# Kernel optimization log

Hardware: AMD Instinct MI355X
Metric: run time of the kernel (lower is better)

The kernel has to match this reference:

```python
import jax, jax.numpy as jnp
import numpy as np

B, N, D, H = 8, 1024, 512, 512  # batch, nodes/graph, input dim, hidden/output dim
NEG_SLOPE = 0.2


def _gatv2_layer(x, src, dst, Wl, bl, Wr, br, a, bias, nseg):
    """PyG GATv2Conv (heads=1, add_self_loops=False, eval mode -> no dropout).
    message j->i: alpha_ij = softmax_i( a . leaky_relu(xl[j] + xr[i]) ); out[i] = sum_j alpha_ij * xl[j] + bias
    """
    xl = x @ Wl + bl              # [nseg, H] source transform
    xr = x @ Wr + br              # [nseg, H] target transform
    e = jax.nn.leaky_relu(xl[src] + xr[dst], NEG_SLOPE) @ a  # [E] raw scores
    m = jax.lax.stop_gradient(jax.ops.segment_max(e, dst, num_segments=nseg))
    ex = jnp.exp(e - m[dst])
    s = jax.ops.segment_sum(ex, dst, num_segments=nseg)
    alpha = ex / s[dst]                                       # segment softmax over incoming edges
    out = jax.ops.segment_sum(alpha[:, None] * xl[src], dst, num_segments=nseg)
    return out + bias


def setup_inputs() -> dict:
    key = jax.random.key(0)
    rng = np.random.RandomState(0)
    # random per-graph adjacency, avg degree ~16; block-diagonal edge extraction
    adj_np = (rng.rand(B, N, N) < (16.0 / N))
    srcs, dsts = [], []
    for b in range(B):  # matches torch.nonzero(big_adj).t(): row=src, col=dst
        r, c = np.nonzero(adj_np[b])
        srcs.append(r + b * N)
        dsts.append(c + b * N)
    edge_index = jnp.asarray(np.stack([np.concatenate(srcs), np.concatenate(dsts)]).astype(np.int32))

    ks = jax.random.split(key, 32)
    def lin(k, fi, fo):
        return (jax.random.normal(k, (fi, fo), jnp.float32) / np.sqrt(fi)).astype(jnp.float32)
    inp = {
        "batch_graph": jax.random.normal(ks[0], (B, N, D), jnp.float32),
        "adj": jnp.asarray(adj_np.astype(np.float32)),
        "edge_index": edge_index,
    }
    dims = [(D, H), (H, H), (H, H)]
    for i, (fi, fo) in enumerate(dims, start=1):
        k = jax.random.split(ks[i], 6)
        inp[f"Wl{i}"] = lin(k[0], fi, fo)
        inp[f"bl{i}"] = jnp.zeros((fo,), jnp.float32)
        inp[f"Wr{i}"] = lin(k[1], fi, fo)
        inp[f"br{i}"] = jnp.zeros((fo,), jnp.float32)
        inp[f"a{i}"] = (jax.random.normal(k[2], (fo,), jnp.float32) / np.sqrt(fo)).astype(jnp.float32)
        inp[f"bias{i}"] = jnp.zeros((fo,), jnp.float32)
    return inp


def reference(batch_graph, adj, edge_index,
              Wl1, bl1, Wr1, br1, a1, bias1,
              Wl2, bl2, Wr2, br2, a2, bias2,
              Wl3, bl3, Wr3, br3, a3, bias3):
    b, n, d = batch_graph.shape
    nseg = b * n
    x = batch_graph.reshape(nseg, d)
    src, dst = edge_index[0], edge_index[1]
    x = _gatv2_layer(x, src, dst, Wl1, bl1, Wr1, br1, a1, bias1, nseg)  # graph_norm = Identity
    x = _gatv2_layer(x, src, dst, Wl2, bl2, Wr2, br2, a2, bias2, nseg)
    x = _gatv2_layer(x, src, dst, Wl3, bl3, Wr3, br3, a3, bias3, nseg)
    return x.reshape(b, n, -1)
```

## Files before the change

### kernel.cpp

```cpp
#include <hip/hip_runtime.h>
#include <math.h>

#define MTOT 8192
#define HD   512

typedef __attribute__((ext_vector_type(8))) short bf16x8;
typedef __attribute__((ext_vector_type(4))) float floatx4;

__device__ inline unsigned short f2bf(float f) {
    unsigned int u = __float_as_uint(f);
    unsigned int r = (u + 0x7FFFu + ((u >> 16) & 1u)) >> 16;
    return (unsigned short)r;
}
__device__ inline float bf2f(unsigned short h) {
    return __uint_as_float(((unsigned int)h) << 16);
}

__device__ inline float wave_sum64(float v) {
    int t;
    t = __builtin_amdgcn_update_dpp(0, __float_as_int(v), 0x121, 0xF, 0xF, true); v += __int_as_float(t);
    t = __builtin_amdgcn_update_dpp(0, __float_as_int(v), 0x122, 0xF, 0xF, true); v += __int_as_float(t);
    t = __builtin_amdgcn_update_dpp(0, __float_as_int(v), 0x124, 0xF, 0xF, true); v += __int_as_float(t);
    t = __builtin_amdgcn_update_dpp(0, __float_as_int(v), 0x128, 0xF, 0xF, true); v += __int_as_float(t);
    v += __shfl_xor(v, 16, 64);
    v += __shfl_xor(v, 32, 64);
    return v;
}


__global__ void count_deg(const int* __restrict__ dst, int* __restrict__ deg, int E) {
    int i = blockIdx.x * 256 + threadIdx.x;
    if (i < E) atomicAdd(&deg[dst[i]], 1);
}

__global__ __launch_bounds__(1024) void scan_offsets(const int* __restrict__ deg,
                                                     int* __restrict__ offs,
                                                     int* __restrict__ cursor) {
    __shared__ int part[1024];
    int tid = threadIdx.x;
    int base = tid * 8;
    int v[8]; int s = 0;
    #pragma unroll
    for (int i = 0; i < 8; ++i) { v[i] = deg[base + i]; s += v[i]; }
    part[tid] = s;
    __syncthreads();
    for (int off = 1; off < 1024; off <<= 1) {
        int t = (tid >= off) ? part[tid - off] : 0;
        __syncthreads();
        part[tid] += t;
        __syncthreads();
    }
    int run = (tid == 0) ? 0 : part[tid - 1];
    #pragma unroll
    for (int i = 0; i < 8; ++i) {
        offs[base + i] = run;
        cursor[base + i] = run;
        run += v[i];
    }
    if (tid == 1023) offs[MTOT] = run;
}

__global__ void scatter_edges(const int* __restrict__ src, const int* __restrict__ dst,
                              int* __restrict__ cursor, int* __restrict__ csr_src, int E) {
    int i = blockIdx.x * 256 + threadIdx.x;
    if (i < E) {
        int p = atomicAdd(&cursor[dst[i]], 1);
        csr_src[p] = src[i];
    }
}


__global__ __launch_bounds__(256) void prep_convert(
    const float* __restrict__ W0, const float* __restrict__ W1,
    const float* __restrict__ W2, const float* __restrict__ W3,
    const float* __restrict__ W4, const float* __restrict__ W5,
    unsigned short* __restrict__ wtbase,
    const float* __restrict__ X,
    unsigned short* __restrict__ Ahi, unsigned short* __restrict__ Alo,
    int* __restrict__ deg)
{
    int z = blockIdx.z;
    if (z == 7) {
        if (blockIdx.x == 0 && blockIdx.y == 0)
            for (int i = threadIdx.x; i < MTOT; i += 256) deg[i] = 0;
        return;
    }
    if (z == 6) {
        int bid = blockIdx.x * 16 + blockIdx.y;
        int t0 = bid * 256 + threadIdx.x;
        #pragma unroll
        for (int it = 0; it < 16; ++it) {
            int i = (t0 + it * 65536) * 4;
            float4 vv = *(const float4*)(X + i);
            ushort4 h, l;
            h.x = f2bf(vv.x); l.x = f2bf(vv.x - bf2f(h.x));
            h.y = f2bf(vv.y); l.y = f2bf(vv.y - bf2f(h.y));
            h.z = f2bf(vv.z); l.z = f2bf(vv.z - bf2f(h.z));
            h.w = f2bf(vv.w); l.w = f2bf(vv.w - bf2f(h.w));
            *(ushort4*)(Ahi + i) = h;
            *(ushort4*)(Alo + i) = l;
        }
        return;
    }
    const float* W = (z == 0) ? W0 : (z == 1) ? W1 : (z == 2) ? W2
                   : (z == 3) ? W3 : (z == 4) ? W4 : W5;
    int L = z >> 1, lr = z & 1;
    const size_t SZ = (size_t)HD * HD;
    unsigned short* Whi = wtbase + (L * 4 + lr * 2) * SZ;
    unsigned short* Wlo = Whi + SZ;

    __shared__ float t[32][33];
    int bx = blockIdx.x * 32;
    int by = blockIdx.y * 32;
    int tx = threadIdx.x & 31, ty = threadIdx.x >> 5;
    for (int i = ty; i < 32; i += 8)
        t[i][tx] = W[(size_t)(by + i) * HD + bx + tx];
    __syncthreads();
    for (int i = ty; i < 32; i += 8) {
        float vv = t[tx][i];
        unsigned short h = f2bf(vv);
        unsigned short l = f2bf(vv - bf2f(h));
        Whi[(size_t)(bx + i) * HD + by + tx] = h;
        Wlo[(size_t)(bx + i) * HD + by + tx] = l;
    }
}


__global__ __launch_bounds__(256) void gemm_mfma_dual(
    const unsigned short* __restrict__ Ahi, const unsigned short* __restrict__ Alo,
    const unsigned short* __restrict__ Bhi_l, const unsigned short* __restrict__ Blo_l,
    const unsigned short* __restrict__ Bhi_r, const unsigned short* __restrict__ Blo_r,
    const float* __restrict__ bias_l, const float* __restrict__ bias_r,
    float* __restrict__ Cl, float* __restrict__ Cr)
{
    int bid = blockIdx.x;
    int virt = (bid & 7) * 64 + (bid >> 3);
    int g  = virt >> 3;
    int q  = virt & 7;
    int bz = q >> 2;
    int bm = g * 128, bn = (q & 3) * 128;

    const unsigned short* Bhi = bz ? Bhi_r : Bhi_l;
    const unsigned short* Blo = bz ? Blo_r : Blo_l;
    const float* bias         = bz ? bias_r : bias_l;
    float* C                  = bz ? Cr : Cl;

    __shared__ __align__(16) unsigned short lds[2][4 * 128 * 32];

    int tid = threadIdx.x;
    int wave = tid >> 6, lane = tid & 63;

    const unsigned short* gsrc[4] = {Ahi, Alo, Bhi, Blo};
    int rowbase[4] = {bm, bm, bn, bn};

    const unsigned short* gbase =
        gsrc[wave] + (size_t)(rowbase[wave] + (lane >> 2)) * 512 + (lane & 3) * 8;

    floatx4 acc[4][4] = {};

    int wm = wave & 1, wn = wave >> 1;
    int lr = lane & 15, lq = lane >> 4;

    #pragma unroll
    for (int rg = 0; rg < 8; ++rg) {
        __builtin_amdgcn_global_load_lds(
            (const __attribute__((address_space(1))) unsigned int*)(gbase + (size_t)rg * 16 * 512),
            (__attribute__((address_space(3))) unsigned int*)(&lds[0][wave * 4096 + rg * 512]),
            16, 0, 0);
    }
    __syncthreads();

    for (int it = 0; it < 16; ++it) {
        int cur = it & 1;
        if (it < 15) {
            const unsigned short* g2 = gbase + (it + 1) * 32;
            #pragma unroll
            for (int rg = 0; rg < 8; ++rg) {
                __builtin_amdgcn_global_load_lds(
                    (const __attribute__((address_space(1))) unsigned int*)(g2 + (size_t)rg * 16 * 512),
                    (__attribute__((address_space(3))) unsigned int*)(&lds[cur ^ 1][wave * 4096 + rg * 512]),
                    16, 0, 0);
            }
        }

        bf16x8 ah[4], al[4], bh[4], bl_[4];
        #pragma unroll
        for (int i = 0; i < 4; ++i) {
            int mrow = wm * 64 + i * 16 + lr;
            ah[i]  = *(const bf16x8*)&lds[cur][0 * 4096 + mrow * 32 + lq * 8];
            al[i]  = *(const bf16x8*)&lds[cur][1 * 4096 + mrow * 32 + lq * 8];
            int nrow = wn * 64 + i * 16 + lr;
            bh[i]  = *(const bf16x8*)&lds[cur][2 * 4096 + nrow * 32 + lq * 8];
            bl_[i] = *(const bf16x8*)&lds[cur][3 * 4096 + nrow * 32 + lq * 8];
        }
        #pragma unroll
        for (int i = 0; i < 4; ++i)
            #pragma unroll
            for (int j = 0; j < 4; ++j) {
                acc[i][j] = __builtin_amdgcn_mfma_f32_16x16x32_bf16(ah[i], bh[j],  acc[i][j], 0, 0, 0);
                acc[i][j] = __builtin_amdgcn_mfma_f32_16x16x32_bf16(ah[i], bl_[j], acc[i][j], 0, 0, 0);
                acc[i][j] = __builtin_amdgcn_mfma_f32_16x16x32_bf16(al[i], bh[j],  acc[i][j], 0, 0, 0);
            }

        __syncthreads();
    }

    #pragma unroll
    for (int j = 0; j < 4; ++j) {
        int n = bn + wn * 64 + j * 16 + lr;
        float bv = bias[n];
        #pragma unroll
        for (int i = 0; i < 4; ++i) {
            int mbase = bm + wm * 64 + i * 16 + lq * 4;
            #pragma unroll
            for (int r = 0; r < 4; ++r)
                C[(size_t)(mbase + r) * 512 + n] = acc[i][j][r] + bv;
        }
    }
}


#define DOT8(Xa, Xb, d0, d1)                                              \
    {                                                                     \
        float t_;                                                         \
        t_ = Xa.x + r0.x; d0 = fmaf(av0.x, t_, d0); d1 = fmaf(av0.x, fabsf(t_), d1); \
        t_ = Xa.y + r0.y; d0 = fmaf(av0.y, t_, d0); d1 = fmaf(av0.y, fabsf(t_), d1); \
        t_ = Xa.z + r0.z; d0 = fmaf(av0.z, t_, d0); d1 = fmaf(av0.z, fabsf(t_), d1); \
        t_ = Xa.w + r0.w; d0 = fmaf(av0.w, t_, d0); d1 = fmaf(av0.w, fabsf(t_), d1); \
        t_ = Xb.x + r1.x; d0 = fmaf(av1.x, t_, d0); d1 = fmaf(av1.x, fabsf(t_), d1); \
        t_ = Xb.y + r1.y; d0 = fmaf(av1.y, t_, d0); d1 = fmaf(av1.y, fabsf(t_), d1); \
        t_ = Xb.z + r1.z; d0 = fmaf(av1.z, t_, d0); d1 = fmaf(av1.z, fabsf(t_), d1); \
        t_ = Xb.w + r1.w; d0 = fmaf(av1.w, t_, d0); d1 = fmaf(av1.w, fabsf(t_), d1); \
    }

#define PROCESS4(Xa, Xb, q)                                               \
    {                                                                     \
        float pe[4];                                                      \
        _Pragma("unroll")                                                 \
        for (int k2 = 0; k2 < 4; ++k2) {                                  \
            float d0 = 0.f, d1 = 0.f;                                     \
            DOT8(Xa[k2], Xb[k2], d0, d1);                                 \
            pe[k2] = fmaf(0.6f, d0, 0.4f * d1);                           \
        }                                                                 \
        _Pragma("unroll")                                                 \
        for (int k2 = 0; k2 < 4; ++k2) pe[k2] = wave_sum64(pe[k2]);       \
        float e0 = pe[0];                                                 \
        float e1 = ((q) + 1 < ne) ? pe[1] : -3.0e38f;                     \
        float e2 = ((q) + 2 < ne) ? pe[2] : -3.0e38f;                     \
        float e3 = ((q) + 3 < ne) ? pe[3] : -3.0e38f;                     \
        float bm4 = fmaxf(fmaxf(e0, e1), fmaxf(e2, e3));                  \
        if (bm4 > m) {                                                    \
            float sc = __expf(m - bm4);                                   \
            s *= sc;                                                      \
            acc0.x *= sc; acc0.y *= sc; acc0.z *= sc; acc0.w *= sc;       \
            acc1.x *= sc; acc1.y *= sc; acc1.z *= sc; acc1.w *= sc;       \
            m = bm4;                                                      \
        }                                                                 \
        float w0 = __expf(e0 - m), w1 = __expf(e1 - m);                   \
        float w2 = __expf(e2 - m), w3 = __expf(e3 - m);                   \
        s += (w0 + w1) + (w2 + w3);                                       \
        acc0.x = fmaf(w0, Xa[0].x, fmaf(w1, Xa[1].x, fmaf(w2, Xa[2].x, fmaf(w3, Xa[3].x, acc0.x)))); \
        acc0.y = fmaf(w0, Xa[0].y, fmaf(w1, Xa[1].y, fmaf(w2, Xa[2].y, fmaf(w3, Xa[3].y, acc0.y)))); \
        acc0.z = fmaf(w0, Xa[0].z, fmaf(w1, Xa[1].z, fmaf(w2, Xa[2].z, fmaf(w3, Xa[3].z, acc0.z)))); \
        acc0.w = fmaf(w0, Xa[0].w, fmaf(w1, Xa[1].w, fmaf(w2, Xa[2].w, fmaf(w3, Xa[3].w, acc0.w)))); \
        acc1.x = fmaf(w0, Xb[0].x, fmaf(w1, Xb[1].x, fmaf(w2, Xb[2].x, fmaf(w3, Xb[3].x, acc1.x)))); \
        acc1.y = fmaf(w0, Xb[0].y, fmaf(w1, Xb[1].y, fmaf(w2, Xb[2].y, fmaf(w3, Xb[3].y, acc1.y)))); \
        acc1.z = fmaf(w0, Xb[0].z, fmaf(w1, Xb[1].z, fmaf(w2, Xb[2].z, fmaf(w3, Xb[3].z, acc1.z)))); \
        acc1.w = fmaf(w0, Xb[0].w, fmaf(w1, Xb[1].w, fmaf(w2, Xb[2].w, fmaf(w3, Xb[3].w, acc1.w)))); \
    }

__global__ __launch_bounds__(256, 4) void gat_online(
    const float* __restrict__ xl, const float* __restrict__ xr,
    const float* __restrict__ avec, const float* __restrict__ bias,
    const int* __restrict__ offs, const int* __restrict__ csr_src,
    float* __restrict__ out, unsigned short* __restrict__ Ohi,
    unsigned short* __restrict__ Olo, int write_fp32)
{
    int gid = blockIdx.x;
    int wv = threadIdx.x >> 6, lane = threadIdx.x & 63;
    int node = ((gid & 7) << 10) + ((gid >> 3) << 2) + wv;

    int nb = offs[node], ne = offs[node + 1];

    int jA[4], jB[4];
    int j0 = (nb < ne) ? csr_src[nb] : 0;
    jA[0] = j0;
    #pragma unroll
    for (int k = 1; k < 4; ++k) jA[k] = (nb + k < ne) ? csr_src[nb + k] : j0;
    #pragma unroll
    for (int k = 0; k < 4; ++k) jB[k] = (nb + 4 + k < ne) ? csr_src[nb + 4 + k] : j0;

    size_t loff = (size_t)lane * 8;
    size_t rowoff = (size_t)node * HD + loff;
    float4 r0 = *(const float4*)(xr + rowoff);
    float4 r1 = *(const float4*)(xr + rowoff + 4);
    float4 av0 = *(const float4*)(avec + loff);
    float4 av1 = *(const float4*)(avec + loff + 4);

    float m = -3.0e38f, s = 0.f;
    float4 acc0 = {0.f, 0.f, 0.f, 0.f}, acc1 = {0.f, 0.f, 0.f, 0.f};

    float4 Aa[4], Ab[4], Ba[4], Bb[4];
    #pragma unroll
    for (int k = 0; k < 4; ++k) {
        const float* xp = xl + (size_t)jA[k] * HD + loff;
        Aa[k] = *(const float4*)xp;
        Ab[k] = *(const float4*)(xp + 4);
    }

    int p = nb;
    if (p < ne) {
        for (;;) {
            #pragma unroll
            for (int k = 0; k < 4; ++k) {
                const float* xp = xl + (size_t)jB[k] * HD + loff;
                Ba[k] = *(const float4*)xp;
                Bb[k] = *(const float4*)(xp + 4);
            }
            {
                int p2 = p + 8;
                #pragma unroll
                for (int k = 0; k < 4; ++k)
                    jA[k] = (p2 + k < ne) ? csr_src[p2 + k] : j0;
            }
            PROCESS4(Aa, Ab, p);
            p += 4;
            if (p >= ne) break;

            #pragma unroll
            for (int k = 0; k < 4; ++k) {
                const float* xp = xl + (size_t)jA[k] * HD + loff;
                Aa[k] = *(const float4*)xp;
                Ab[k] = *(const float4*)(xp + 4);
            }
            {
                int p2 = p + 8;
                #pragma unroll
                for (int k = 0; k < 4; ++k)
                    jB[k] = (p2 + k < ne) ? csr_src[p2 + k] : j0;
            }
            PROCESS4(Ba, Bb, p);
            p += 4;
            if (p >= ne) break;
        }
    }

    float inv = (s > 0.f) ? 1.f / s : 0.f;
    float4 b0 = *(const float4*)(bias + loff);
    float4 b1 = *(const float4*)(bias + loff + 4);
    float4 o0, o1;
    o0.x = fmaf(acc0.x, inv, b0.x); o0.y = fmaf(acc0.y, inv, b0.y);
    o0.z = fmaf(acc0.z, inv, b0.z); o0.w = fmaf(acc0.w, inv, b0.w);
    o1.x = fmaf(acc1.x, inv, b1.x); o1.y = fmaf(acc1.y, inv, b1.y);
    o1.z = fmaf(acc1.z, inv, b1.z); o1.w = fmaf(acc1.w, inv, b1.w);

    if (write_fp32) {
        *(float4*)(out + rowoff) = o0;
        *(float4*)(out + rowoff + 4) = o1;
    } else {
        ushort4 h, lo;
        h.x = f2bf(o0.x); lo.x = f2bf(o0.x - bf2f(h.x));
        h.y = f2bf(o0.y); lo.y = f2bf(o0.y - bf2f(h.y));
        h.z = f2bf(o0.z); lo.z = f2bf(o0.z - bf2f(h.z));
        h.w = f2bf(o0.w); lo.w = f2bf(o0.w - bf2f(h.w));
        *(ushort4*)(Ohi + rowoff) = h;
        *(ushort4*)(Olo + rowoff) = lo;
        h.x = f2bf(o1.x); lo.x = f2bf(o1.x - bf2f(h.x));
        h.y = f2bf(o1.y); lo.y = f2bf(o1.y - bf2f(h.y));
        h.z = f2bf(o1.z); lo.z = f2bf(o1.z - bf2f(h.z));
        h.w = f2bf(o1.w); lo.w = f2bf(o1.w - bf2f(h.w));
        *(ushort4*)(Ohi + rowoff + 4) = h;
        *(ushort4*)(Olo + rowoff + 4) = lo;
    }
}


extern "C" void kernel_launch(void* const* d_in, const int* in_sizes, int n_in,
                              void* d_out, int out_size, void* d_ws, size_t ws_size,
                              hipStream_t stream) {
    const float* x0 = (const float*)d_in[0];
    const int* eidx = (const int*)d_in[2];
    int E = in_sizes[2] / 2;
    const int* esrc = eidx;
    const int* edst = eidx + E;

    const float* Wl[3] = {(const float*)d_in[3],  (const float*)d_in[9],  (const float*)d_in[15]};
    const float* bl[3] = {(const float*)d_in[4],  (const float*)d_in[10], (const float*)d_in[16]};
    const float* Wr[3] = {(const float*)d_in[5],  (const float*)d_in[11], (const float*)d_in[17]};
    const float* br[3] = {(const float*)d_in[6],  (const float*)d_in[12], (const float*)d_in[18]};
    const float* av[3] = {(const float*)d_in[7],  (const float*)d_in[13], (const float*)d_in[19]};
    const float* bs[3] = {(const float*)d_in[8],  (const float*)d_in[14], (const float*)d_in[20]};

    char* w = (char*)d_ws;
    unsigned short* Ahi = (unsigned short*)w; w += (size_t)MTOT * HD * 2;
    unsigned short* Alo = (unsigned short*)w; w += (size_t)MTOT * HD * 2;
    unsigned short* wtbase = (unsigned short*)w; w += 12 * (size_t)HD * HD * 2;
    float* xl = (float*)w; w += (size_t)MTOT * HD * 4;
    float* xr = (float*)w; w += (size_t)MTOT * HD * 4;
    int* deg    = (int*)w;
    int* offs   = deg + MTOT;
    int* cursor = offs + MTOT + 8;
    int* csr    = cursor + MTOT;
    const size_t SZ = (size_t)HD * HD;

    prep_convert<<<dim3(16, 16, 8), 256, 0, stream>>>(
        Wl[0], Wr[0], Wl[1], Wr[1], Wl[2], Wr[2], wtbase, x0, Ahi, Alo, deg);
    count_deg<<<(E + 255) / 256, 256, 0, stream>>>(edst, deg, E);
    scan_offsets<<<1, 1024, 0, stream>>>(deg, offs, cursor);
    scatter_edges<<<(E + 255) / 256, 256, 0, stream>>>(esrc, edst, cursor, csr, E);

    for (int L = 0; L < 3; ++L) {
        gemm_mfma_dual<<<512, 256, 0, stream>>>(Ahi, Alo,
            wtbase + (L * 4 + 0) * SZ, wtbase + (L * 4 + 1) * SZ,
            wtbase + (L * 4 + 2) * SZ, wtbase + (L * 4 + 3) * SZ,
            bl[L], br[L], xl, xr);
        int last = (L == 2);
        gat_online<<<MTOT / 4, 256, 0, stream>>>(xl, xr, av[L], bs[L], offs, csr,
                                                 last ? (float*)d_out : nullptr,
                                                 last ? nullptr : Ahi,
                                                 last ? nullptr : Alo,
                                                 last);
    }
}
```

Measured before the change: 305.7 us.

## Process two destination nodes per wave in GAT aggregation, interleaving their edge streams

The online-softmax aggregation kernel now assigns two destination nodes to each wave instead of one, alternating 4-edge chunks between the two nodes so that one node's gathers can overlap the other's compute. The grid is halved and the launch-bounds occupancy hint drops from 4 to 3 to allow for the extra registers. Each node's prefetch is now single-buffered rather than double-buffered, and the added register pressure lowers occupancy, which may cancel the gain from the added instruction-level parallelism.

```diff
diff --git a/kernel.cpp b/kernel.cpp
--- a/kernel.cpp
+++ b/kernel.cpp
@@ -220,56 +220,84 @@
 }
 
 
-#define DOT8(Xa, Xb, d0, d1)                                              \
+#define DOT8P(Xa, Xb, Ra, Rb, d0, d1)                                     \
     {                                                                     \
         float t_;                                                         \
-        t_ = Xa.x + r0.x; d0 = fmaf(av0.x, t_, d0); d1 = fmaf(av0.x, fabsf(t_), d1); \
-        t_ = Xa.y + r0.y; d0 = fmaf(av0.y, t_, d0); d1 = fmaf(av0.y, fabsf(t_), d1); \
-        t_ = Xa.z + r0.z; d0 = fmaf(av0.z, t_, d0); d1 = fmaf(av0.z, fabsf(t_), d1); \
-        t_ = Xa.w + r0.w; d0 = fmaf(av0.w, t_, d0); d1 = fmaf(av0.w, fabsf(t_), d1); \
-        t_ = Xb.x + r1.x; d0 = fmaf(av1.x, t_, d0); d1 = fmaf(av1.x, fabsf(t_), d1); \
-        t_ = Xb.y + r1.y; d0 = fmaf(av1.y, t_, d0); d1 = fmaf(av1.y, fabsf(t_), d1); \
-        t_ = Xb.z + r1.z; d0 = fmaf(av1.z, t_, d0); d1 = fmaf(av1.z, fabsf(t_), d1); \
-        t_ = Xb.w + r1.w; d0 = fmaf(av1.w, t_, d0); d1 = fmaf(av1.w, fabsf(t_), d1); \
-    }
-
-#define PROCESS4(Xa, Xb, q)                                               \
+        t_ = Xa.x + Ra.x; d0 = fmaf(av0.x, t_, d0); d1 = fmaf(av0.x, fabsf(t_), d1); \
+        t_ = Xa.y + Ra.y; d0 = fmaf(av0.y, t_, d0); d1 = fmaf(av0.y, fabsf(t_), d1); \
+        t_ = Xa.z + Ra.z; d0 = fmaf(av0.z, t_, d0); d1 = fmaf(av0.z, fabsf(t_), d1); \
+        t_ = Xa.w + Ra.w; d0 = fmaf(av0.w, t_, d0); d1 = fmaf(av0.w, fabsf(t_), d1); \
+        t_ = Xb.x + Rb.x; d0 = fmaf(av1.x, t_, d0); d1 = fmaf(av1.x, fabsf(t_), d1); \
+        t_ = Xb.y + Rb.y; d0 = fmaf(av1.y, t_, d0); d1 = fmaf(av1.y, fabsf(t_), d1); \
+        t_ = Xb.z + Rb.z; d0 = fmaf(av1.z, t_, d0); d1 = fmaf(av1.z, fabsf(t_), d1); \
+        t_ = Xb.w + Rb.w; d0 = fmaf(av1.w, t_, d0); d1 = fmaf(av1.w, fabsf(t_), d1); \
+    }
+
+#define PROC4(Xa, Xb, q, NE, M, S, A0, A1, Ra, Rb)                        \
     {                                                                     \
         float pe[4];                                                      \
         _Pragma("unroll")                                                 \
         for (int k2 = 0; k2 < 4; ++k2) {                                  \
             float d0 = 0.f, d1 = 0.f;                                     \
-            DOT8(Xa[k2], Xb[k2], d0, d1);                                 \
+            DOT8P(Xa[k2], Xb[k2], Ra, Rb, d0, d1);                        \
             pe[k2] = fmaf(0.6f, d0, 0.4f * d1);                           \
         }                                                                 \
         _Pragma("unroll")                                                 \
         for (int k2 = 0; k2 < 4; ++k2) pe[k2] = wave_sum64(pe[k2]);       \
         float e0 = pe[0];                                                 \
-        float e1 = ((q) + 1 < ne) ? pe[1] : -3.0e38f;                     \
-        float e2 = ((q) + 2 < ne) ? pe[2] : -3.0e38f;                     \
-        float e3 = ((q) + 3 < ne) ? pe[3] : -3.0e38f;                     \
+        float e1 = ((q) + 1 < (NE)) ? pe[1] : -3.0e38f;                   \
+        float e2 = ((q) + 2 < (NE)) ? pe[2] : -3.0e38f;                   \
+        float e3 = ((q) + 3 < (NE)) ? pe[3] : -3.0e38f;                   \
         float bm4 = fmaxf(fmaxf(e0, e1), fmaxf(e2, e3));                  \
-        if (bm4 > m) {                                                    \
-            float sc = __expf(m - bm4);                                   \
-            s *= sc;                                                      \
-            acc0.x *= sc; acc0.y *= sc; acc0.z *= sc; acc0.w *= sc;       \
-            acc1.x *= sc; acc1.y *= sc; acc1.z *= sc; acc1.w *= sc;       \
-            m = bm4;                                                      \
+        if (bm4 > (M)) {                                                  \
+            float sc = __expf((M) - bm4);                                 \
+            (S) *= sc;                                                    \
+            A0.x *= sc; A0.y *= sc; A0.z *= sc; A0.w *= sc;               \
+            A1.x *= sc; A1.y *= sc; A1.z *= sc; A1.w *= sc;               \
+            (M) = bm4;                                                    \
         }                                                                 \
-        float w0 = __expf(e0 - m), w1 = __expf(e1 - m);                   \
-        float w2 = __expf(e2 - m), w3 = __expf(e3 - m);                   \
-        s += (w0 + w1) + (w2 + w3);                                       \
-        acc0.x = fmaf(w0, Xa[0].x, fmaf(w1, Xa[1].x, fmaf(w2, Xa[2].x, fmaf(w3, Xa[3].x, acc0.x)))); \
-        acc0.y = fmaf(w0, Xa[0].y, fmaf(w1, Xa[1].y, fmaf(w2, Xa[2].y, fmaf(w3, Xa[3].y, acc0.y)))); \
-        acc0.z = fmaf(w0, Xa[0].z, fmaf(w1, Xa[1].z, fmaf(w2, Xa[2].z, fmaf(w3, Xa[3].z, acc0.z)))); \
-        acc0.w = fmaf(w0, Xa[0].w, fmaf(w1, Xa[1].w, fmaf(w2, Xa[2].w, fmaf(w3, Xa[3].w, acc0.w)))); \
-        acc1.x = fmaf(w0, Xb[0].x, fmaf(w1, Xb[1].x, fmaf(w2, Xb[2].x, fmaf(w3, Xb[3].x, acc1.x)))); \
-        acc1.y = fmaf(w0, Xb[0].y, fmaf(w1, Xb[1].y, fmaf(w2, Xb[2].y, fmaf(w3, Xb[3].y, acc1.y)))); \
-        acc1.z = fmaf(w0, Xb[0].z, fmaf(w1, Xb[1].z, fmaf(w2, Xb[2].z, fmaf(w3, Xb[3].z, acc1.z)))); \
-        acc1.w = fmaf(w0, Xb[0].w, fmaf(w1, Xb[1].w, fmaf(w2, Xb[2].w, fmaf(w3, Xb[3].w, acc1.w)))); \
-    }
-
-__global__ __launch_bounds__(256, 4) void gat_online(
+        float w0 = __expf(e0 - (M)), w1 = __expf(e1 - (M));               \
+        float w2 = __expf(e2 - (M)), w3 = __expf(e3 - (M));               \
+        (S) += (w0 + w1) + (w2 + w3);                                     \
+        A0.x = fmaf(w0, Xa[0].x, fmaf(w1, Xa[1].x, fmaf(w2, Xa[2].x, fmaf(w3, Xa[3].x, A0.x)))); \
+        A0.y = fmaf(w0, Xa[0].y, fmaf(w1, Xa[1].y, fmaf(w2, Xa[2].y, fmaf(w3, Xa[3].y, A0.y)))); \
+        A0.z = fmaf(w0, Xa[0].z, fmaf(w1, Xa[1].z, fmaf(w2, Xa[2].z, fmaf(w3, Xa[3].z, A0.z)))); \
+        A0.w = fmaf(w0, Xa[0].w, fmaf(w1, Xa[1].w, fmaf(w2, Xa[2].w, fmaf(w3, Xa[3].w, A0.w)))); \
+        A1.x = fmaf(w0, Xb[0].x, fmaf(w1, Xb[1].x, fmaf(w2, Xb[2].x, fmaf(w3, Xb[3].x, A1.x)))); \
+        A1.y = fmaf(w0, Xb[0].y, fmaf(w1, Xb[1].y, fmaf(w2, Xb[2].y, fmaf(w3, Xb[3].y, A1.y)))); \
+        A1.z = fmaf(w0, Xb[0].z, fmaf(w1, Xb[1].z, fmaf(w2, Xb[2].z, fmaf(w3, Xb[3].z, A1.z)))); \
+        A1.w = fmaf(w0, Xb[0].w, fmaf(w1, Xb[1].w, fmaf(w2, Xb[2].w, fmaf(w3, Xb[3].w, A1.w)))); \
+    }
+
+#define STORE_NODE(ROWOFF, A0, A1, S)                                     \
+    {                                                                     \
+        float inv = ((S) > 0.f) ? 1.f / (S) : 0.f;                        \
+        float4 o0, o1;                                                    \
+        o0.x = fmaf(A0.x, inv, b0.x); o0.y = fmaf(A0.y, inv, b0.y);       \
+        o0.z = fmaf(A0.z, inv, b0.z); o0.w = fmaf(A0.w, inv, b0.w);       \
+        o1.x = fmaf(A1.x, inv, b1.x); o1.y = fmaf(A1.y, inv, b1.y);       \
+        o1.z = fmaf(A1.z, inv, b1.z); o1.w = fmaf(A1.w, inv, b1.w);       \
+        if (write_fp32) {                                                 \
+            *(float4*)(out + (ROWOFF)) = o0;                              \
+            *(float4*)(out + (ROWOFF) + 4) = o1;                          \
+        } else {                                                          \
+            ushort4 h, lo;                                                \
+            h.x = f2bf(o0.x); lo.x = f2bf(o0.x - bf2f(h.x));              \
+            h.y = f2bf(o0.y); lo.y = f2bf(o0.y - bf2f(h.y));              \
+            h.z = f2bf(o0.z); lo.z = f2bf(o0.z - bf2f(h.z));              \
+            h.w = f2bf(o0.w); lo.w = f2bf(o0.w - bf2f(h.w));              \
+            *(ushort4*)(Ohi + (ROWOFF)) = h;                              \
+            *(ushort4*)(Olo + (ROWOFF)) = lo;                             \
+            h.x = f2bf(o1.x); lo.x = f2bf(o1.x - bf2f(h.x));              \
+            h.y = f2bf(o1.y); lo.y = f2bf(o1.y - bf2f(h.y));              \
+            h.z = f2bf(o1.z); lo.z = f2bf(o1.z - bf2f(h.z));              \
+            h.w = f2bf(o1.w); lo.w = f2bf(o1.w - bf2f(h.w));              \
+            *(ushort4*)(Ohi + (ROWOFF) + 4) = h;                          \
+            *(ushort4*)(Olo + (ROWOFF) + 4) = lo;                         \
+        }                                                                 \
+    }
+
+__global__ __launch_bounds__(256, 3) void gat_online(
     const float* __restrict__ xl, const float* __restrict__ xr,
     const float* __restrict__ avec, const float* __restrict__ bias,
     const int* __restrict__ offs, const int* __restrict__ csr_src,
@@ -278,100 +306,97 @@
 {
     int gid = blockIdx.x;
     int wv = threadIdx.x >> 6, lane = threadIdx.x & 63;
-    int node = ((gid & 7) << 10) + ((gid >> 3) << 2) + wv;
-
-    int nb = offs[node], ne = offs[node + 1];
-
-    int jA[4], jB[4];
-    int j0 = (nb < ne) ? csr_src[nb] : 0;
-    jA[0] = j0;
-    #pragma unroll
-    for (int k = 1; k < 4; ++k) jA[k] = (nb + k < ne) ? csr_src[nb + k] : j0;
-    #pragma unroll
-    for (int k = 0; k < 4; ++k) jB[k] = (nb + 4 + k < ne) ? csr_src[nb + 4 + k] : j0;
+    int n0 = ((gid & 7) << 10) + ((gid >> 3) << 3) + wv * 2;
+    int n1 = n0 + 1;
+
+    int nb0 = offs[n0], ne0 = offs[n0 + 1];
+    int nb1 = offs[n1], ne1 = offs[n1 + 1];
+
+    int j0c = (nb0 < ne0) ? csr_src[nb0] : 0;
+    int j1c = (nb1 < ne1) ? csr_src[nb1] : 0;
+    int i0[4], i1[4];
+    i0[0] = j0c; i1[0] = j1c;
+    #pragma unroll
+    for (int k = 1; k < 4; ++k) {
+        i0[k] = (nb0 + k < ne0) ? csr_src[nb0 + k] : j0c;
+        i1[k] = (nb1 + k < ne1) ? csr_src[nb1 + k] : j1c;
+    }
 
     size_t loff = (size_t)lane * 8;
-    size_t rowoff = (size_t)node * HD + loff;
-    float4 r0 = *(const float4*)(xr + rowoff);
-    float4 r1 = *(const float4*)(xr + rowoff + 4);
+    size_t row0 = (size_t)n0 * HD + loff;
+    size_t row1 = (size_t)n1 * HD + loff;
+    float4 r0a = *(const float4*)(xr + row0);
+    float4 r0b = *(const float4*)(xr + row0 + 4);
+    float4 r1a = *(const float4*)(xr + row1);
+    float4 r1b = *(const float4*)(xr + row1 + 4);
     float4 av0 = *(const float4*)(avec + loff);
     float4 av1 = *(const float4*)(avec + loff + 4);
 
-    float m = -3.0e38f, s = 0.f;
-    float4 acc0 = {0.f, 0.f, 0.f, 0.f}, acc1 = {0.f, 0.f, 0.f, 0.f};
-
-    float4 Aa[4], Ab[4], Ba[4], Bb[4];
+    float4 X0a[4], X0b[4], X1a[4], X1b[4];
     #pragma unroll
     for (int k = 0; k < 4; ++k) {
-        const float* xp = xl + (size_t)jA[k] * HD + loff;
-        Aa[k] = *(const float4*)xp;
-        Ab[k] = *(const float4*)(xp + 4);
-    }
-
-    int p = nb;
-    if (p < ne) {
-        for (;;) {
-            #pragma unroll
-            for (int k = 0; k < 4; ++k) {
-                const float* xp = xl + (size_t)jB[k] * HD + loff;
-                Ba[k] = *(const float4*)xp;
-                Bb[k] = *(const float4*)(xp + 4);
-            }
-            {
-                int p2 = p + 8;
+        const float* xp = xl + (size_t)i0[k] * HD + loff;
+        X0a[k] = *(const float4*)xp;
+        X0b[k] = *(const float4*)(xp + 4);
+    }
+    #pragma unroll
+    for (int k = 0; k < 4; ++k) {
+        const float* xp = xl + (size_t)i1[k] * HD + loff;
+        X1a[k] = *(const float4*)xp;
+        X1b[k] = *(const float4*)(xp + 4);
+    }
+
+    int jn0[4], jn1[4];
+    #pragma unroll
+    for (int k = 0; k < 4; ++k) {
+        jn0[k] = (nb0 + 4 + k < ne0) ? csr_src[nb0 + 4 + k] : j0c;
+        jn1[k] = (nb1 + 4 + k < ne1) ? csr_src[nb1 + 4 + k] : j1c;
+    }
+
+    float m0 = -3.0e38f, s0 = 0.f, m1 = -3.0e38f, s1 = 0.f;
+    float4 a00 = {0,0,0,0}, a01 = {0,0,0,0};
+    float4 a10 = {0,0,0,0}, a11 = {0,0,0,0};
+
+    int p0 = nb0, p1 = nb1;
+    while (p0 < ne0 || p1 < ne1) {
+        if (p0 < ne0) {
+            PROC4(X0a, X0b, p0, ne0, m0, s0, a00, a01, r0a, r0b);
+            p0 += 4;
+            if (p0 < ne0) {
+                #pragma unroll
+                for (int k = 0; k < 4; ++k) {
+                    const float* xp = xl + (size_t)jn0[k] * HD + loff;
+                    X0a[k] = *(const float4*)xp;
+                    X0b[k] = *(const float4*)(xp + 4);
+                }
+                int p2 = p0 + 4;
                 #pragma unroll
                 for (int k = 0; k < 4; ++k)
-                    jA[k] = (p2 + k < ne) ? csr_src[p2 + k] : j0;
+                    jn0[k] = (p2 + k < ne0) ? csr_src[p2 + k] : j0c;
             }
-            PROCESS4(Aa, Ab, p);
-            p += 4;
-            if (p >= ne) break;
-
-            #pragma unroll
-            for (int k = 0; k < 4; ++k) {
-                const float* xp = xl + (size_t)jA[k] * HD + loff;
-                Aa[k] = *(const float4*)xp;
-                Ab[k] = *(const float4*)(xp + 4);
-            }
-            {
-                int p2 = p + 8;
+        }
+        if (p1 < ne1) {
+            PROC4(X1a, X1b, p1, ne1, m1, s1, a10, a11, r1a, r1b);
+            p1 += 4;
+            if (p1 < ne1) {
+                #pragma unroll
+                for (int k = 0; k < 4; ++k) {
+                    const float* xp = xl + (size_t)jn1[k] * HD + loff;
+                    X1a[k] = *(const float4*)xp;
+                    X1b[k] = *(const float4*)(xp + 4);
+                }
+                int p2 = p1 + 4;
                 #pragma unroll
                 for (int k = 0; k < 4; ++k)
-                    jB[k] = (p2 + k < ne) ? csr_src[p2 + k] : j0;
+                    jn1[k] = (p2 + k < ne1) ? csr_src[p2 + k] : j1c;
             }
-            PROCESS4(Ba, Bb, p);
-            p += 4;
-            if (p >= ne) break;
-        }
-    }
-
-    float inv = (s > 0.f) ? 1.f / s : 0.f;
+        }
+    }
+
     float4 b0 = *(const float4*)(bias + loff);
     float4 b1 = *(const float4*)(bias + loff + 4);
-    float4 o0, o1;
-    o0.x = fmaf(acc0.x, inv, b0.x); o0.y = fmaf(acc0.y, inv, b0.y);
-    o0.z = fmaf(acc0.z, inv, b0.z); o0.w = fmaf(acc0.w, inv, b0.w);
-    o1.x = fmaf(acc1.x, inv, b1.x); o1.y = fmaf(acc1.y, inv, b1.y);
-    o1.z = fmaf(acc1.z, inv, b1.z); o1.w = fmaf(acc1.w, inv, b1.w);
-
-    if (write_fp32) {
-        *(float4*)(out + rowoff) = o0;
-        *(float4*)(out + rowoff + 4) = o1;
-    } else {
-        ushort4 h, lo;
-        h.x = f2bf(o0.x); lo.x = f2bf(o0.x - bf2f(h.x));
-        h.y = f2bf(o0.y); lo.y = f2bf(o0.y - bf2f(h.y));
-        h.z = f2bf(o0.z); lo.z = f2bf(o0.z - bf2f(h.z));
-        h.w = f2bf(o0.w); lo.w = f2bf(o0.w - bf2f(h.w));
-        *(ushort4*)(Ohi + rowoff) = h;
-        *(ushort4*)(Olo + rowoff) = lo;
-        h.x = f2bf(o1.x); lo.x = f2bf(o1.x - bf2f(h.x));
-        h.y = f2bf(o1.y); lo.y = f2bf(o1.y - bf2f(h.y));
-        h.z = f2bf(o1.z); lo.z = f2bf(o1.z - bf2f(h.z));
-        h.w = f2bf(o1.w); lo.w = f2bf(o1.w - bf2f(h.w));
-        *(ushort4*)(Ohi + rowoff + 4) = h;
-        *(ushort4*)(Olo + rowoff + 4) = lo;
-    }
+    STORE_NODE(row0, a00, a01, s0);
+    STORE_NODE(row1, a10, a11, s1);
 }
 
 
@@ -415,7 +440,7 @@
             wtbase + (L * 4 + 2) * SZ, wtbase + (L * 4 + 3) * SZ,
             bl[L], br[L], xl, xr);
         int last = (L == 2);
-        gat_online<<<MTOT / 4, 256, 0, stream>>>(xl, xr, av[L], bs[L], offs, csr,
+        gat_online<<<MTOT / 8, 256, 0, stream>>>(xl, xr, av[L], bs[L], offs, csr,
                                                  last ? (float*)d_out : nullptr,
                                                  last ? nullptr : Ahi,
                                                  last ? nullptr : Alo,
```

Result: no change. 311.4 us (+1.9%).
